# Kernel optimization log

Hardware: AMD Instinct MI355X
Metric: run time of the kernel (lower is better)

## Reference

```python
import jax, jax.numpy as jnp
import numpy as np

NUM_AA = 20
NUM_PAIRS = NUM_AA * NUM_AA  # 400 k-spaced amino-acid pair buckets


def setup_inputs() -> dict:
    key = jax.random.key(0)
    k1, k2 = jax.random.split(key)
    B, L, D = 256, 2048, 64
    seq = jax.random.randint(k1, (B, L), 0, NUM_AA, dtype=jnp.int64 if jax.config.jax_enable_x64 else jnp.int32)
    emb = jax.random.normal(k2, (B, L, D), dtype=jnp.float32)
    return {"seq": seq, "emb": emb, "k": 3}


def reference(seq, emb, k):
    """Vectorized CKSAAP embedding code.

    seq: [B, L] int amino-acid indices in [0, 20)
    emb: [B, L, D] float per-residue embeddings
    Returns: [B, k+1, 20, 20, D] averaged pair embeddings, matching
    CKSAAP.return_CKSAAP_Emb_code applied to each sequence in the batch.
    """
    B, L = seq.shape
    D = emb.shape[-1]

    def per_seq(s, e):
        outs = []
        for t in range(k + 1):
            n = L - t - 1  # number of k-spaced pairs for this gap
            left = s[:n]
            right = s[t + 1 : t + 1 + n]
            idx = left * NUM_AA + right  # [n] pair bucket index
            vals = 0.5 * (e[:n] + e[t + 1 : t + 1 + n])  # [n, D]
            hist = jax.ops.segment_sum(vals, idx, num_segments=NUM_PAIRS)  # [400, D]
            outs.append((hist / float(n)).reshape(NUM_AA, NUM_AA, D))
        return jnp.stack(outs)  # [k+1, 20, 20, D]

    return jax.vmap(per_seq)(seq, emb)
```

## Files before the change

kernel.cpp:

```cpp
#include <hip/hip_runtime.h>
#include <hip/hip_bf16.h>

#define NUM_AA    20
#define NUM_PAIRS 400
#define DD        64
#define NT        512
#define NW        8
#define GB        8
#define LMAX      2048

__global__ __launch_bounds__(NT, 4)
void cksaap_kernel(const int* __restrict__ seq,
                   const float* __restrict__ emb,
                   float* __restrict__ out,
                   int B, int L, int k)
{
    __shared__ int            s_seq[LMAX];
    __shared__ unsigned short s_idx[LMAX];
    __shared__ unsigned short s_ord[LMAX];
    __shared__ unsigned short s_bkt[NUM_PAIRS];
    __shared__ int            s_cnt[NUM_PAIRS];
    __shared__ int            s_off[NUM_PAIRS];
    __shared__ int            s_cur[NUM_PAIRS];
    __shared__ int            s_scan[NT];
    __shared__ int            s_chist[64];
    __shared__ int            s_coff[64];

    const int T   = k + 1;
    const int nwg = gridDim.x;
    const int i   = blockIdx.x;
    int b, t;
    if (nwg == 1024 && T == 4) {
        const int x = i & 7;
        const int s = i >> 3;
        t = s >> 5;
        b = x * 32 + (s & 31);
    } else {
        b = i / T; t = i % T;
    }

    const int tid  = threadIdx.x;
    const int lane = tid & 63;
    const int wave = tid >> 6;
    const int n    = L - t - 1;

    for (int j = tid; j < L; j += NT) s_seq[j] = seq[(size_t)b * L + j];
    if (tid < NUM_PAIRS) s_cnt[tid] = 0;
    if (tid < 64) s_chist[tid] = 0;
    __syncthreads();

    for (int j = tid; j < n; j += NT) {
        const int idx = s_seq[j] * NUM_AA + s_seq[j + t + 1];
        s_idx[j] = (unsigned short)idx;
        atomicAdd(&s_cnt[idx], 1);
    }
    __syncthreads();

    const int c0 = (tid < NUM_PAIRS) ? s_cnt[tid] : 0;
    s_scan[tid] = c0;
    __syncthreads();
    for (int off = 1; off < NT; off <<= 1) {
        int v = s_scan[tid];
        if (tid >= off) v += s_scan[tid - off];
        __syncthreads();
        s_scan[tid] = v;
        __syncthreads();
    }
    if (tid < NUM_PAIRS) {
        const int excl = s_scan[tid] - c0;
        s_off[tid] = excl;
        s_cur[tid] = excl;
    }
    if (tid < NUM_PAIRS) atomicAdd(&s_chist[min(c0, 63)], 1);
    __syncthreads();

    for (int j = tid; j < n; j += NT) {
        const int idx = s_idx[j];
        const int r   = atomicAdd(&s_cur[idx], 1);
        s_ord[r] = (unsigned short)j;
    }
    if (tid < 64) {
        int s = 0;
        for (int c2 = tid + 1; c2 < 64; ++c2) s += s_chist[c2];
        s_coff[tid] = s;
    }
    __syncthreads();
    if (tid < NUM_PAIRS) {
        const int r = atomicAdd(&s_coff[min(s_cnt[tid], 63)], 1);
        s_bkt[r] = (unsigned short)tid;
    }
    __syncthreads();

    const float  scale = 0.5f / (float)n;
    const float* embb  = emb + (size_t)b * L * DD;
    float*       outp  = out + ((size_t)b * T + t) * (size_t)(NUM_PAIRS * DD);
    const int    gap   = (t + 1) * DD;
    const int    ngroups = NUM_PAIRS / GB;

    for (int g = wave; g < ngroups; g += NW) {
        const int r0 = g * GB;
        int pid[GB], cc[GB], off[GB];
        #pragma unroll
        for (int q = 0; q < GB; ++q) {
            pid[q] = s_bkt[r0 + q];
            cc[q]  = s_cnt[pid[q]];
            off[q] = s_off[pid[q]];
        }
        int gmax = 0;
        #pragma unroll
        for (int q = 0; q < GB; ++q) gmax = max(gmax, cc[q]);

        float acc[GB];
        #pragma unroll
        for (int q = 0; q < GB; ++q) acc[q] = 0.0f;

        for (int m = 0; m < gmax; ++m) {
            #pragma unroll
            for (int q = 0; q < GB; ++q) {
                const bool  ok = (m < cc[q]);
                const int   j  = ok ? (int)s_ord[off[q] + m] : 0;
                const float w  = ok ? 1.0f : 0.0f;
                const float a  = embb[(size_t)j * DD + lane];
                const float bb = embb[(size_t)j * DD + gap + lane];
                acc[q] += w * (a + bb);
            }
        }

        #pragma unroll
        for (int q = 0; q < GB; ++q) {
            outp[(size_t)pid[q] * DD + lane] = acc[q] * scale;
        }
    }
}

extern "C" void kernel_launch(void* const* d_in, const int* in_sizes, int n_in,
                              void* d_out, int out_size, void* d_ws, size_t ws_size,
                              hipStream_t stream)
{
    const int*   seq = (const int*)d_in[0];
    const float* emb = (const float*)d_in[1];
    float*       out = (float*)d_out;

    const int B = 256;
    const int L = in_sizes[0] / B;
    const int k = out_size / (B * NUM_PAIRS * DD) - 1;

    cksaap_kernel<<<B * (k + 1), NT, 0, stream>>>(seq, emb, out, B, L, k);
}
```

Baseline: 323.2 us.

## Gather pair sums with float4 loads, one pair per 16-lane quarter

```diff
diff --git a/kernel.cpp b/kernel.cpp
--- a/kernel.cpp
+++ b/kernel.cpp
@@ -6,10 +6,11 @@
 #define DD        64
 #define NT        512
 #define NW        8
-#define GB        8
 #define LMAX      2048
 
-__global__ __launch_bounds__(NT, 4)
+typedef float f4 __attribute__((ext_vector_type(4)));
+
+__global__ __launch_bounds__(NT, 8)
 void cksaap_kernel(const int* __restrict__ seq,
                    const float* __restrict__ emb,
                    float* __restrict__ out,
@@ -70,8 +71,8 @@
         const int excl = s_scan[tid] - c0;
         s_off[tid] = excl;
         s_cur[tid] = excl;
+        atomicAdd(&s_chist[min(c0, 63)], 1);
     }
-    if (tid < NUM_PAIRS) atomicAdd(&s_chist[min(c0, 63)], 1);
     __syncthreads();
 
     for (int j = tid; j < n; j += NT) {
@@ -91,45 +92,45 @@
     }
     __syncthreads();
 
-    const float  scale = 0.5f / (float)n;
-    const float* embb  = emb + (size_t)b * L * DD;
-    float*       outp  = out + ((size_t)b * T + t) * (size_t)(NUM_PAIRS * DD);
-    const int    gap   = (t + 1) * DD;
-    const int    ngroups = NUM_PAIRS / GB;
+    const float  scale   = 0.5f / (float)n;
+    const float* embb    = emb + (size_t)b * L * DD;
+    float*       outp    = out + ((size_t)b * T + t) * (size_t)(NUM_PAIRS * DD);
+    const int    gap     = (t + 1) * DD;
+    const int    quarter = lane >> 4;
+    const int    dlo     = (lane & 15) * 4;
 
-    for (int g = wave; g < ngroups; g += NW) {
-        const int r0 = g * GB;
-        int pid[GB], cc[GB], off[GB];
-        #pragma unroll
-        for (int q = 0; q < GB; ++q) {
-            pid[q] = s_bkt[r0 + q];
-            cc[q]  = s_cnt[pid[q]];
-            off[q] = s_off[pid[q]];
+    for (int g = wave; g < NUM_PAIRS / 4; g += NW) {
+        const int r0  = g * 4;
+        const int pid = s_bkt[r0 + quarter];
+        const int cc  = s_cnt[pid];
+        const int off = s_off[pid];
+        const int gmax = s_cnt[s_bkt[r0]];
+
+        f4 acc = {0.0f, 0.0f, 0.0f, 0.0f};
+        int m = 0;
+        for (; m + 2 <= gmax; m += 2) {
+            const bool  ok0 = (m     < cc);
+            const bool  ok1 = (m + 1 < cc);
+            const int   j0  = ok0 ? (int)s_ord[off + m]     : 0;
+            const int   j1  = ok1 ? (int)s_ord[off + m + 1] : 0;
+            const float w0  = ok0 ? 1.0f : 0.0f;
+            const float w1  = ok1 ? 1.0f : 0.0f;
+            const f4 a0 = *(const f4*)&embb[(size_t)j0 * DD + dlo];
+            const f4 b0 = *(const f4*)&embb[(size_t)j0 * DD + gap + dlo];
+            const f4 a1 = *(const f4*)&embb[(size_t)j1 * DD + dlo];
+            const f4 b1 = *(const f4*)&embb[(size_t)j1 * DD + gap + dlo];
+            acc += w0 * (a0 + b0) + w1 * (a1 + b1);
         }
-        int gmax = 0;
-        #pragma unroll
-        for (int q = 0; q < GB; ++q) gmax = max(gmax, cc[q]);
-
-        float acc[GB];
-        #pragma unroll
-        for (int q = 0; q < GB; ++q) acc[q] = 0.0f;
-
-        for (int m = 0; m < gmax; ++m) {
-            #pragma unroll
-            for (int q = 0; q < GB; ++q) {
-                const bool  ok = (m < cc[q]);
-                const int   j  = ok ? (int)s_ord[off[q] + m] : 0;
-                const float w  = ok ? 1.0f : 0.0f;
-                const float a  = embb[(size_t)j * DD + lane];
-                const float bb = embb[(size_t)j * DD + gap + lane];
-                acc[q] += w * (a + bb);
-            }
+        if (m < gmax) {
+            const bool  ok0 = (m < cc);
+            const int   j0  = ok0 ? (int)s_ord[off + m] : 0;
+            const float w0  = ok0 ? 1.0f : 0.0f;
+            const f4 a0 = *(const f4*)&embb[(size_t)j0 * DD + dlo];
+            const f4 b0 = *(const f4*)&embb[(size_t)j0 * DD + gap + dlo];
+            acc += w0 * (a0 + b0);
         }
 
-        #pragma unroll
-        for (int q = 0; q < GB; ++q) {
-            outp[(size_t)pid[q] * DD + lane] = acc[q] * scale;
-        }
+        *(f4*)&outp[(size_t)pid * DD + dlo] = acc * scale;
     }
 }
 
```

New measurement: 324.2 us. Within noise of the previous version (+0.3%).
